# Optimization experiments

Measured on AMD Instinct MI355X. Metric: run time of the kernel, lower is better.

## Reference

```python
import math
import jax, jax.numpy as jnp
import numpy as np

B, T, D = 8, 1024, 1152
H = 16
E = 4  # expansion factor
EPS = 1e-6


def setup_inputs() -> dict:
    key = jax.random.key(0)
    ks = jax.random.split(key, 12)
    std = 0.02
    return {
        "x": jax.random.normal(ks[0], (B, T, D), dtype=jnp.float32),
        "c": jax.random.normal(ks[1], (B, D), dtype=jnp.float32),
        # weights stored [in, out]
        "qkv_w": jax.random.normal(ks[2], (D, 3 * D), dtype=jnp.float32) * std,
        "qkv_b": jnp.zeros((3 * D,), dtype=jnp.float32),
        "out_w": jax.random.normal(ks[3], (D, D), dtype=jnp.float32) * std,
        "out_b": jnp.zeros((D,), dtype=jnp.float32),
        "w1": jax.random.normal(ks[4], (D, E * D), dtype=jnp.float32) * std,
        "b1": jnp.zeros((E * D,), dtype=jnp.float32),
        "w2": jax.random.normal(ks[5], (E * D, D), dtype=jnp.float32) * std,
        "b2": jnp.zeros((D,), dtype=jnp.float32),
        "ada_w": jax.random.normal(ks[6], (D, 6 * D), dtype=jnp.float32) * std,
        "ada_b": jnp.zeros((6 * D,), dtype=jnp.float32),
    }


def _layer_norm(x):
    mu = jnp.mean(x, axis=-1, keepdims=True)
    var = jnp.mean(jnp.square(x - mu), axis=-1, keepdims=True)
    return (x - mu) * jax.lax.rsqrt(var + EPS)


def _modulate(x, shift, scale):
    return x * (1.0 + scale) + shift


def _attention(y, qkv_w, qkv_b, out_w, out_b):
    b, t, d = y.shape
    hd = d // H
    qkv = y @ qkv_w + qkv_b                      # [B,T,3D]
    q, k, v = jnp.split(qkv, 3, axis=-1)
    q = q.reshape(b, t, H, hd).transpose(0, 2, 1, 3)  # [B,H,T,hd]
    k = k.reshape(b, t, H, hd).transpose(0, 2, 1, 3)
    v = v.reshape(b, t, H, hd).transpose(0, 2, 1, 3)
    scores = jnp.einsum("bhqd,bhkd->bhqk", q, k) / math.sqrt(hd)
    attn = jax.nn.softmax(scores, axis=-1)
    out = jnp.einsum("bhqk,bhkd->bhqd", attn, v)      # [B,H,T,hd]
    out = out.transpose(0, 2, 1, 3).reshape(b, t, d)
    return out @ out_w + out_b


def reference(x, c, qkv_w, qkv_b, out_w, out_b, w1, b1, w2, b2, ada_w, ada_b):
    mods = (jax.nn.silu(c) @ ada_w + ada_b)[:, None, :]     # [B,1,6D]
    m0, m1, m2, m3, m4, m5 = jnp.split(mods, 6, axis=-1)
    y = _modulate(_layer_norm(x), m0, m1)
    x = x + m2 * _attention(y, qkv_w, qkv_b, out_w, out_b)
    y = _modulate(_layer_norm(x), m3, m4)
    y = jax.nn.gelu(y @ w1 + b1, approximate=True)
    x = x + m5 * (y @ w2 + b2)
    return x
```

## Files before the change

### kernel.cpp

```cpp
#include <hip/hip_runtime.h>

#define B_ 8
#define T_ 1024
#define D_ 1152
#define H_ 16
#define HD_ 72
#define M_ (B_*T_)
#define D3_ (3*D_)
#define D4_ (4*D_)
#define D6_ (6*D_)

#define DP_ 96
#define QB_ 64
#define KB_ 32
#define KP_ 104
#define VP_ 40

typedef unsigned short u16;
typedef __attribute__((ext_vector_type(4))) float f32x4;
typedef __attribute__((ext_vector_type(4))) unsigned int u32x4;

__device__ __forceinline__ u16 f2b(float f) {
  union { float f; unsigned u; } v; v.f = f;
  unsigned r = v.u + 0x7FFFu + ((v.u >> 16) & 1u);
  return (u16)(r >> 16);
}
__device__ __forceinline__ float b2f(u16 h) {
  union { unsigned u; float f; } v; v.u = ((unsigned)h) << 16;
  return v.f;
}

__device__ __forceinline__ void mfma16x16x32(f32x4& d, u32x4 a, u32x4 b) {
  asm("v_mfma_f32_16x16x32_bf16 %0, %1, %2, %0" : "+v"(d) : "v"(a), "v"(b));
}

__device__ __forceinline__ void load_lds16(const void* g, void* l) {
  __builtin_amdgcn_global_load_lds((const __attribute__((address_space(1))) void*)g,
                                   (__attribute__((address_space(3))) void*)l, 16, 0, 0);
}

__global__ __launch_bounds__(256) void wconv_kernel(const float* __restrict__ W,
                                                    u16* __restrict__ Wt, int K, int N) {
  __shared__ float tile[32][33];
  int k0 = blockIdx.y * 32, n0 = blockIdx.x * 32;
  int tx = threadIdx.x, ty = threadIdx.y;
  #pragma unroll
  for (int i = 0; i < 32; i += 8)
    tile[ty + i][tx] = W[(size_t)(k0 + ty + i) * N + n0 + tx];
  __syncthreads();
  #pragma unroll
  for (int i = 0; i < 32; i += 8)
    Wt[(size_t)(n0 + ty + i) * K + k0 + tx] = f2b(tile[tx][ty + i]);
}

__global__ __launch_bounds__(256) void mods_kernel(const float* __restrict__ c,
                                                   const float* __restrict__ ada_w,
                                                   const float* __restrict__ ada_b,
                                                   float* __restrict__ mods) {
  int b = blockIdx.x;
  int j = blockIdx.y * 256 + threadIdx.x;
  __shared__ float sc[D_];
  for (int d = threadIdx.x; d < D_; d += 256) {
    float v = c[b * D_ + d];
    sc[d] = v / (1.f + __expf(-v));
  }
  __syncthreads();
  float acc = ada_b[j];
  for (int k = 0; k < D_; ++k) acc += sc[k] * ada_w[(size_t)k * D6_ + j];
  mods[b * D6_ + j] = acc;
}

__global__ __launch_bounds__(256) void ln_mod_kernel(const float* __restrict__ x,
                                                     const float* __restrict__ mods,
                                                     int shift_off, int scale_off,
                                                     u16* __restrict__ y) {
  int row = blockIdx.x;
  int b = row >> 10;
  int tid = threadIdx.x;
  const float* xr = x + (size_t)row * D_;
  float s = 0.f, ss = 0.f;
  for (int d = tid; d < D_; d += 256) { float v = xr[d]; s += v; ss += v * v; }
  #pragma unroll
  for (int o = 32; o > 0; o >>= 1) { s += __shfl_down(s, o); ss += __shfl_down(ss, o); }
  __shared__ float red[2][4];
  int wid = tid >> 6, lane = tid & 63;
  if (lane == 0) { red[0][wid] = s; red[1][wid] = ss; }
  __syncthreads();
  __shared__ float stat[2];
  if (tid == 0) {
    float S = red[0][0] + red[0][1] + red[0][2] + red[0][3];
    float SS = red[1][0] + red[1][1] + red[1][2] + red[1][3];
    float mu = S * (1.f / D_);
    float var = SS * (1.f / D_) - mu * mu;
    stat[0] = mu; stat[1] = rsqrtf(var + 1e-6f);
  }
  __syncthreads();
  float mu = stat[0], inv = stat[1];
  const float* sh = mods + b * D6_ + shift_off;
  const float* scl = mods + b * D6_ + scale_off;
  u16* yr = y + (size_t)row * D_;
  for (int d = tid; d < D_; d += 256) {
    float v = (xr[d] - mu) * inv;
    yr[d] = f2b(v * (1.f + scl[d]) + sh[d]);
  }
}

template<int EPI>
__global__ __launch_bounds__(256, 2)
void gemm_kernel(const u16* __restrict__ A, const u16* __restrict__ Bt,
                 const float* __restrict__ bias, const float* __restrict__ resid,
                 const float* __restrict__ mods, int mod_off,
                 void* __restrict__ Cout, u16* __restrict__ q_out,
                 u16* __restrict__ k_out, u16* __restrict__ v_out, int N, int K) {
  __shared__ __align__(16) u16 As[128 * 32];
  __shared__ __align__(16) u16 Bs[128 * 32];
  int bm = blockIdx.x, bn = blockIdx.y;
  int tid = threadIdx.x;
  int lane = tid & 63;
  int wid = tid >> 6;
  int wm = wid >> 1, wn = wid & 1;
  int fr = lane & 15, fq = lane >> 4;

  f32x4 acc[4][4] = {};

  const char* Ab = (const char*)A + (size_t)bm * 128 * K * 2;
  const char* Bb = (const char*)Bt + (size_t)bn * 128 * K * 2;
  int o0 = tid * 16;
  int r0 = o0 >> 6, cb = o0 & 63;
  const char* Ag0 = Ab + (size_t)r0 * (K * 2) + cb;
  const char* Ag1 = Ab + (size_t)(r0 + 64) * (K * 2) + cb;
  const char* Bg0 = Bb + (size_t)r0 * (K * 2) + cb;
  const char* Bg1 = Bb + (size_t)(r0 + 64) * (K * 2) + cb;
  u16* Al0 = As + (o0 >> 1);
  u16* Al1 = As + ((o0 + 4096) >> 1);
  u16* Bl0 = Bs + (o0 >> 1);
  u16* Bl1 = Bs + ((o0 + 4096) >> 1);

  const u32x4* pA = ((const u32x4*)As) + (wm * 64 + fr) * 4 + fq;
  const u32x4* pB = ((const u32x4*)Bs) + (wn * 64 + fr) * 4 + fq;

  for (int k0 = 0; k0 < K; k0 += 32) {
    size_t kb = (size_t)k0 * 2;
    load_lds16(Ag0 + kb, Al0);
    load_lds16(Ag1 + kb, Al1);
    load_lds16(Bg0 + kb, Bl0);
    load_lds16(Bg1 + kb, Bl1);
    __syncthreads();
    u32x4 af[4], bfr[4];
    #pragma unroll
    for (int m = 0; m < 4; ++m) af[m] = pA[m * 64];
    #pragma unroll
    for (int n = 0; n < 4; ++n) bfr[n] = pB[n * 64];
    #pragma unroll
    for (int m = 0; m < 4; ++m)
      #pragma unroll
      for (int n = 0; n < 4; ++n)
        mfma16x16x32(acc[m][n], af[m], bfr[n]);
    __syncthreads();
  }

  #pragma unroll
  for (int m = 0; m < 4; ++m) {
    int grb = bm * 128 + wm * 64 + m * 16 + fq * 4;
    #pragma unroll
    for (int n = 0; n < 4; ++n) {
      int gc = bn * 128 + wn * 64 + n * 16 + fr;
      float bv = bias[gc];
      #pragma unroll
      for (int j = 0; j < 4; ++j) {
        int gr = grb + j;
        size_t idx = (size_t)gr * N + gc;
        float v = acc[m][n][j] + bv;
        if (EPI == 0) {
          ((u16*)Cout)[idx] = f2b(v);
        } else if (EPI == 1) {
          float g = v / (1.f + __expf(-1.5957691216f * (v + 0.044715f * v * v * v)));
          ((u16*)Cout)[idx] = f2b(g);
        } else if (EPI == 2) {
          int b = gr >> 10;
          float mv = mods[b * D6_ + mod_off + gc];
          ((float*)Cout)[idx] = resid[idx] + mv * v;
        } else {
          int b = gr >> 10, t = gr & 1023;
          int sec = gc / D_;
          int rem = gc - sec * D_;
          int h = rem / HD_;
          int d = rem - h * HD_;
          size_t hbrow = ((size_t)b * H_ + h) * T_ + t;
          u16 bv16 = f2b(v);
          if (sec == 0)      q_out[hbrow * DP_ + d] = bv16;
          else if (sec == 1) k_out[hbrow * DP_ + d] = bv16;
          else               v_out[hbrow * HD_ + d] = bv16;
        }
      }
    }
  }
}

__global__ __launch_bounds__(256, 2) void attn_mfma_kernel(
    const u16* __restrict__ qbuf, const u16* __restrict__ kbuf,
    const u16* __restrict__ vbuf, u16* __restrict__ attn_out) {
  int qt = blockIdx.x, h = blockIdx.y, b = blockIdx.z;
  int tid = threadIdx.x;
  int lane = tid & 63, wid = tid >> 6;
  int fr = lane & 15, g = lane >> 4;

  __shared__ __align__(16) u16 Qs[QB_ * KP_];
  __shared__ __align__(16) u16 Ks[KB_ * KP_];
  __shared__ __align__(16) u16 Vt[80 * VP_];
  __shared__ __align__(16) u16 Ps[4][16 * VP_];
  __shared__ float arow[4][16];
  __shared__ float lrow[4][16];

  const size_t hb = ((size_t)b * H_ + h) * T_;
  int q0 = qt * QB_;

  for (int c = tid; c < QB_ * 12; c += 256) {
    int r = c / 12, c16 = c % 12;
    *(u32x4*)((char*)Qs + r * (KP_ * 2) + c16 * 16) =
        *(const u32x4*)((const char*)(qbuf + (hb + q0 + r) * DP_) + c16 * 16);
  }
  if (tid < 320) Vt[72 * VP_ + tid] = 0;
  __syncthreads();

  u32x4 qf[3];
  #pragma unroll
  for (int ds = 0; ds < 3; ++ds)
    qf[ds] = *(const u32x4*)((const char*)Qs + (wid * 16 + fr) * (KP_ * 2) + ds * 64 + g * 16);

  float mreg = -1e30f, lreg = 0.f;
  f32x4 acc[5] = {};
  const float scale = 0.11785113019775793f;

  for (int kt = 0; kt < T_ / KB_; ++kt) {
    int k0 = kt * KB_;
    for (int c = tid; c < KB_ * 12; c += 256) {
      int r = c / 12, c16 = c % 12;
      *(u32x4*)((char*)Ks + r * (KP_ * 2) + c16 * 16) =
          *(const u32x4*)((const char*)(kbuf + (hb + k0 + r) * DP_) + c16 * 16);
    }
    for (int u = tid; u < KB_ * HD_; u += 256) {
      int r = u / HD_, d = u - r * HD_;
      Vt[d * VP_ + r] = vbuf[(hb + k0 + r) * HD_ + d];
    }
    __syncthreads();

    f32x4 s0 = {}, s1 = {};
    #pragma unroll
    for (int ds = 0; ds < 3; ++ds) {
      u32x4 k0f = *(const u32x4*)((const char*)Ks + fr * (KP_ * 2) + ds * 64 + g * 16);
      u32x4 k1f = *(const u32x4*)((const char*)Ks + (16 + fr) * (KP_ * 2) + ds * 64 + g * 16);
      mfma16x16x32(s0, k0f, qf[ds]);
      mfma16x16x32(s1, k1f, qf[ds]);
    }
    float mt = -1e30f;
    #pragma unroll
    for (int j = 0; j < 4; ++j) {
      s0[j] *= scale; s1[j] *= scale;
      mt = fmaxf(mt, fmaxf(s0[j], s1[j]));
    }
    mt = fmaxf(mt, __shfl_xor(mt, 16));
    mt = fmaxf(mt, __shfl_xor(mt, 32));
    float mnew = fmaxf(mreg, mt);
    float alpha = __expf(mreg - mnew);
    float psum = 0.f;
    u16* prow = &Ps[wid][fr * VP_];
    #pragma unroll
    for (int j = 0; j < 4; ++j) {
      float p0 = __expf(s0[j] - mnew);
      float p1 = __expf(s1[j] - mnew);
      psum += p0 + p1;
      prow[4 * g + j] = f2b(p0);
      prow[16 + 4 * g + j] = f2b(p1);
    }
    psum += __shfl_xor(psum, 16);
    psum += __shfl_xor(psum, 32);
    lreg = lreg * alpha + psum;
    mreg = mnew;
    if (g == 0) arow[wid][fr] = alpha;
    asm volatile("s_waitcnt lgkmcnt(0)" ::: "memory");
    float al[4];
    #pragma unroll
    for (int j = 0; j < 4; ++j) al[j] = arow[wid][4 * g + j];
    #pragma unroll
    for (int n = 0; n < 5; ++n)
      #pragma unroll
      for (int j = 0; j < 4; ++j) acc[n][j] *= al[j];
    u32x4 pf = *(const u32x4*)((const char*)&Ps[wid][0] + fr * (VP_ * 2) + g * 16);
    #pragma unroll
    for (int n = 0; n < 5; ++n) {
      u32x4 vf = *(const u32x4*)((const char*)Vt + (n * 16 + fr) * (VP_ * 2) + g * 16);
      mfma16x16x32(acc[n], pf, vf);
    }
    __syncthreads();
  }

  if (g == 0) lrow[wid][fr] = lreg;
  asm volatile("s_waitcnt lgkmcnt(0)" ::: "memory");
  float linv[4];
  #pragma unroll
  for (int j = 0; j < 4; ++j) linv[j] = 1.f / lrow[wid][4 * g + j];
  size_t orow_base = (size_t)b * T_ + q0 + wid * 16;
  #pragma unroll
  for (int n = 0; n < 5; ++n) {
    int d = n * 16 + fr;
    if (d < HD_) {
      #pragma unroll
      for (int j = 0; j < 4; ++j)
        attn_out[(orow_base + 4 * g + j) * D_ + h * HD_ + d] = f2b(acc[n][j] * linv[j]);
    }
  }
}

extern "C" void kernel_launch(void* const* d_in, const int* in_sizes, int n_in,
                              void* d_out, int out_size, void* d_ws, size_t ws_size,
                              hipStream_t stream) {
  const float* x     = (const float*)d_in[0];
  const float* c     = (const float*)d_in[1];
  const float* qkv_w = (const float*)d_in[2];
  const float* qkv_b = (const float*)d_in[3];
  const float* out_w = (const float*)d_in[4];
  const float* out_b = (const float*)d_in[5];
  const float* w1    = (const float*)d_in[6];
  const float* b1    = (const float*)d_in[7];
  const float* w2    = (const float*)d_in[8];
  const float* b2    = (const float*)d_in[9];
  const float* ada_w = (const float*)d_in[10];
  const float* ada_b = (const float*)d_in[11];
  float* out = (float*)d_out;

  char* ws = (char*)d_ws;
  size_t off = 0;
  auto alloc = [&](size_t bytes) { void* p = ws + off; off += (bytes + 255) & ~(size_t)255; return p; };
  float* mods   = (float*)alloc((size_t)B_ * D6_ * 4);
  u16* qkv_wt   = (u16*)alloc((size_t)D_ * D3_ * 2);
  u16* out_wt   = (u16*)alloc((size_t)D_ * D_ * 2);
  u16* w1t      = (u16*)alloc((size_t)D_ * D4_ * 2);
  u16* w2t      = (u16*)alloc((size_t)D4_ * D_ * 2);
  u16* ybuf     = (u16*)alloc((size_t)M_ * D_ * 2);
  u16* qbuf     = (u16*)alloc((size_t)B_ * H_ * T_ * DP_ * 2);
  u16* kbuf     = (u16*)alloc((size_t)B_ * H_ * T_ * DP_ * 2);
  u16* vbuf     = (u16*)alloc((size_t)B_ * H_ * T_ * HD_ * 2);
  u16* attnbuf  = (u16*)alloc((size_t)M_ * D_ * 2);
  float* x1     = (float*)alloc((size_t)M_ * D_ * 4);
  u16* h1       = (u16*)alloc((size_t)M_ * D4_ * 2);
  (void)ws_size; (void)in_sizes; (void)n_in; (void)out_size;

  dim3 tb32(32, 8);
  wconv_kernel<<<dim3(D3_ / 32, D_ / 32), tb32, 0, stream>>>(qkv_w, qkv_wt, D_, D3_);
  wconv_kernel<<<dim3(D_ / 32, D_ / 32), tb32, 0, stream>>>(out_w, out_wt, D_, D_);
  wconv_kernel<<<dim3(D4_ / 32, D_ / 32), tb32, 0, stream>>>(w1, w1t, D_, D4_);
  wconv_kernel<<<dim3(D_ / 32, D4_ / 32), tb32, 0, stream>>>(w2, w2t, D4_, D_);

  mods_kernel<<<dim3(B_, D6_ / 256), 256, 0, stream>>>(c, ada_w, ada_b, mods);

  ln_mod_kernel<<<M_, 256, 0, stream>>>(x, mods, 0, D_, ybuf);

  hipMemsetAsync(qbuf, 0, (size_t)B_ * H_ * T_ * DP_ * 2, stream);
  hipMemsetAsync(kbuf, 0, (size_t)B_ * H_ * T_ * DP_ * 2, stream);

  gemm_kernel<3><<<dim3(M_ / 128, D3_ / 128), 256, 0, stream>>>(
      ybuf, qkv_wt, qkv_b, nullptr, nullptr, 0, nullptr, qbuf, kbuf, vbuf, D3_, D_);

  attn_mfma_kernel<<<dim3(T_ / QB_, H_, B_), 256, 0, stream>>>(qbuf, kbuf, vbuf, attnbuf);

  gemm_kernel<2><<<dim3(M_ / 128, D_ / 128), 256, 0, stream>>>(
      attnbuf, out_wt, out_b, x, mods, 2 * D_, x1, nullptr, nullptr, nullptr, D_, D_);

  ln_mod_kernel<<<M_, 256, 0, stream>>>(x1, mods, 3 * D_, 4 * D_, ybuf);

  gemm_kernel<1><<<dim3(M_ / 128, D4_ / 128), 256, 0, stream>>>(
      ybuf, w1t, b1, nullptr, nullptr, 0, h1, nullptr, nullptr, nullptr, D4_, D_);

  gemm_kernel<2><<<dim3(M_ / 128, D_ / 128), 256, 0, stream>>>(
      h1, w2t, b2, x1, mods, 5 * D_, out, nullptr, nullptr, nullptr, D_, D4_);
}
```

Baseline: 918.2 us.

## Double-buffer K/V tiles in attention and store V pre-transposed

The QKV GEMM epilogue now writes V in a [B,H,HD,T] layout, so the attention kernel can load V tiles with 16-byte vector loads instead of element-wise transposing scatter. K and V tiles are double-buffered in shared memory: the next tile is staged while the current one is computed, which removes one barrier per iteration. Q fragments are loaded straight from global memory into registers, skipping the Q shared-memory staging. The risks are scattered strided writes in the GEMM epilogue for V and extra LDS use, which may affect occupancy.

```diff
diff --git a/kernel.cpp b/kernel.cpp
--- a/kernel.cpp
+++ b/kernel.cpp
@@ -15,6 +15,7 @@
 #define KB_ 32
 #define KP_ 104
 #define VP_ 40
+#define NT_ (T_/KB_)
 
 typedef unsigned short u16;
 typedef __attribute__((ext_vector_type(4))) float f32x4;
@@ -186,11 +187,10 @@
           int rem = gc - sec * D_;
           int h = rem / HD_;
           int d = rem - h * HD_;
-          size_t hbrow = ((size_t)b * H_ + h) * T_ + t;
           u16 bv16 = f2b(v);
-          if (sec == 0)      q_out[hbrow * DP_ + d] = bv16;
-          else if (sec == 1) k_out[hbrow * DP_ + d] = bv16;
-          else               v_out[hbrow * HD_ + d] = bv16;
+          if (sec == 0)      q_out[(((size_t)b * H_ + h) * T_ + t) * DP_ + d] = bv16;
+          else if (sec == 1) k_out[(((size_t)b * H_ + h) * T_ + t) * DP_ + d] = bv16;
+          else               v_out[(((size_t)b * H_ + h) * HD_ + d) * T_ + t] = bv16;
         }
       }
     }
@@ -205,51 +205,59 @@
   int lane = tid & 63, wid = tid >> 6;
   int fr = lane & 15, g = lane >> 4;
 
-  __shared__ __align__(16) u16 Qs[QB_ * KP_];
-  __shared__ __align__(16) u16 Ks[KB_ * KP_];
-  __shared__ __align__(16) u16 Vt[80 * VP_];
+  __shared__ __align__(16) u16 Ks[2][KB_ * KP_];
+  __shared__ __align__(16) u16 Vt[2][80 * VP_];
   __shared__ __align__(16) u16 Ps[4][16 * VP_];
   __shared__ float arow[4][16];
   __shared__ float lrow[4][16];
 
   const size_t hb = ((size_t)b * H_ + h) * T_;
+  const size_t vh = ((size_t)b * H_ + h) * HD_ * T_;
   int q0 = qt * QB_;
 
-  for (int c = tid; c < QB_ * 12; c += 256) {
-    int r = c / 12, c16 = c % 12;
-    *(u32x4*)((char*)Qs + r * (KP_ * 2) + c16 * 16) =
-        *(const u32x4*)((const char*)(qbuf + (hb + q0 + r) * DP_) + c16 * 16);
-  }
-  if (tid < 320) Vt[72 * VP_ + tid] = 0;
-  __syncthreads();
-
   u32x4 qf[3];
-  #pragma unroll
-  for (int ds = 0; ds < 3; ++ds)
-    qf[ds] = *(const u32x4*)((const char*)Qs + (wid * 16 + fr) * (KP_ * 2) + ds * 64 + g * 16);
+  {
+    const u16* qrow = qbuf + (hb + q0 + wid * 16 + fr) * DP_;
+    #pragma unroll
+    for (int ds = 0; ds < 3; ++ds)
+      qf[ds] = *(const u32x4*)(qrow + ds * 32 + g * 8);
+  }
+
+  for (int i2 = tid; i2 < 640; i2 += 256)
+    Vt[i2 / 320][72 * VP_ + (i2 % 320)] = 0;
+
+  auto stage = [&](int kt, int p) {
+    int k0 = kt * KB_;
+    const u16* kg = kbuf + (hb + k0) * DP_;
+    const u16* vg = vbuf + vh + k0;
+    for (int c = tid; c < 384 + 288; c += 256) {
+      if (c < 384) {
+        int r = c / 12, c16 = c % 12;
+        *(u32x4*)(Ks[p] + r * KP_ + c16 * 8) = *(const u32x4*)(kg + (size_t)r * DP_ + c16 * 8);
+      } else {
+        int c2 = c - 384;
+        int d = c2 >> 2, cc = c2 & 3;
+        *(u32x4*)(Vt[p] + d * VP_ + cc * 8) = *(const u32x4*)(vg + (size_t)d * T_ + cc * 8);
+      }
+    }
+  };
+
+  stage(0, 0);
+  __syncthreads();
 
   float mreg = -1e30f, lreg = 0.f;
   f32x4 acc[5] = {};
   const float scale = 0.11785113019775793f;
 
-  for (int kt = 0; kt < T_ / KB_; ++kt) {
-    int k0 = kt * KB_;
-    for (int c = tid; c < KB_ * 12; c += 256) {
-      int r = c / 12, c16 = c % 12;
-      *(u32x4*)((char*)Ks + r * (KP_ * 2) + c16 * 16) =
-          *(const u32x4*)((const char*)(kbuf + (hb + k0 + r) * DP_) + c16 * 16);
-    }
-    for (int u = tid; u < KB_ * HD_; u += 256) {
-      int r = u / HD_, d = u - r * HD_;
-      Vt[d * VP_ + r] = vbuf[(hb + k0 + r) * HD_ + d];
-    }
-    __syncthreads();
+  for (int kt = 0; kt < NT_; ++kt) {
+    int p = kt & 1;
+    if (kt + 1 < NT_) stage(kt + 1, p ^ 1);
 
     f32x4 s0 = {}, s1 = {};
     #pragma unroll
     for (int ds = 0; ds < 3; ++ds) {
-      u32x4 k0f = *(const u32x4*)((const char*)Ks + fr * (KP_ * 2) + ds * 64 + g * 16);
-      u32x4 k1f = *(const u32x4*)((const char*)Ks + (16 + fr) * (KP_ * 2) + ds * 64 + g * 16);
+      u32x4 k0f = *(const u32x4*)(Ks[p] + fr * KP_ + ds * 32 + g * 8);
+      u32x4 k1f = *(const u32x4*)(Ks[p] + (16 + fr) * KP_ + ds * 32 + g * 8);
       mfma16x16x32(s0, k0f, qf[ds]);
       mfma16x16x32(s1, k1f, qf[ds]);
     }
@@ -289,7 +297,7 @@
     u32x4 pf = *(const u32x4*)((const char*)&Ps[wid][0] + fr * (VP_ * 2) + g * 16);
     #pragma unroll
     for (int n = 0; n < 5; ++n) {
-      u32x4 vf = *(const u32x4*)((const char*)Vt + (n * 16 + fr) * (VP_ * 2) + g * 16);
+      u32x4 vf = *(const u32x4*)(Vt[p] + (n * 16 + fr) * VP_ + g * 8);
       mfma16x16x32(acc[n], pf, vf);
     }
     __syncthreads();
@@ -340,7 +348,7 @@
   u16* ybuf     = (u16*)alloc((size_t)M_ * D_ * 2);
   u16* qbuf     = (u16*)alloc((size_t)B_ * H_ * T_ * DP_ * 2);
   u16* kbuf     = (u16*)alloc((size_t)B_ * H_ * T_ * DP_ * 2);
-  u16* vbuf     = (u16*)alloc((size_t)B_ * H_ * T_ * HD_ * 2);
+  u16* vbuf     = (u16*)alloc((size_t)B_ * H_ * HD_ * T_ * 2);
   u16* attnbuf  = (u16*)alloc((size_t)M_ * D_ * 2);
   float* x1     = (float*)alloc((size_t)M_ * D_ * 4);
   u16* h1       = (u16*)alloc((size_t)M_ * D4_ * 2);
```

Measured after the change: 793.0 us. 1.16x faster.
